# Kernel tuning notes

Hardware: AMD Instinct MI355X
Metric: run time of the kernel (lower is better)

## Reference

```python
import jax, jax.numpy as jnp
import numpy as np

B, S, H, F, E, R, K = 2, 1024, 2048, 7168, 8, 32, 2


def setup_inputs() -> dict:
    key = jax.random.key(0)
    ks = jax.random.split(key, 12)
    sc = 0.02
    n = lambda k, shape, s: jax.random.normal(k, shape, dtype=jnp.float32) * s
    return {
        "hidden_states": n(ks[0], (B, S, H), 1.0),
        "Wg": n(ks[1], (E, H), sc),          # gate: Linear(H, E)
        "W1": n(ks[2], (F, H), sc),          # shared gate_proj
        "W2": n(ks[3], (H, F), sc),          # shared down_proj
        "W3": n(ks[4], (F, H), sc),          # shared up_proj
        "A1": n(ks[5], (E, R, H), sc),       # per-expert w1_a
        "B1": n(ks[6], (E, F, R), sc),       # per-expert w1_b
        "A2": n(ks[7], (E, R, F), sc),       # per-expert w2_a
        "B2": n(ks[8], (E, H, R), sc),       # per-expert w2_b
        "A3": n(ks[9], (E, R, H), sc),       # per-expert w3_a
        "B3": n(ks[10], (E, F, R), sc),      # per-expert w3_b
    }


def _gather_slot(a_all, e):
    # a_all: [T, E, r], e: [T] -> [T, r]
    return jnp.take_along_axis(a_all, e[:, None, None], axis=1)[:, 0]


def reference(hidden_states, Wg, W1, W2, W3, A1, B1, A2, B2, A3, B3):
    b, s, h = hidden_states.shape
    x = hidden_states.reshape(-1, h)                      # [T, H]
    nE = Wg.shape[0]
    logits = x @ Wg.T                                     # [T, E]
    probs = jax.nn.softmax(logits.astype(jnp.float32), axis=-1)
    rw, sel = jax.lax.top_k(probs, K)                     # [T, K]
    rw = (rw / rw.sum(axis=-1, keepdims=True)).astype(x.dtype)

    # Base projections are shared across experts -> compute once for all tokens.
    base1 = x @ W1.T                                      # [T, F]
    base3 = x @ W3.T                                      # [T, F]
    # Tiny per-expert LoRA down-projections for all tokens ([T, E, R]).
    a1_all = jnp.einsum('th,erh->ter', x, A1)
    a3_all = jnp.einsum('th,erh->ter', x, A3)

    out = jnp.zeros_like(x)
    for k in range(K):  # fixed small loop over top-k slots
        e = sel[:, k]                                     # [T]
        mask = jax.nn.one_hot(e, nE, dtype=x.dtype)       # [T, E]
        a1 = _gather_slot(a1_all, e)                      # [T, R]
        a3 = _gather_slot(a3_all, e)
        lora1 = jnp.einsum('ter,efr->tf', mask[:, :, None] * a1[:, None, :], B1)
        lora3 = jnp.einsum('ter,efr->tf', mask[:, :, None] * a3[:, None, :], B3)
        x1 = base1 + lora1
        x3 = base3 + lora3
        x2 = jax.nn.silu(x1) * x3                         # [T, F]
        down = x2 @ W2.T                                  # [T, H]
        a2_all = jnp.einsum('tf,erf->ter', x2, A2)        # [T, E, R]
        a2 = _gather_slot(a2_all, e)
        lora2 = jnp.einsum('ter,ehr->th', mask[:, :, None] * a2[:, None, :], B2)
        out = out + (down + lora2) * rw[:, k:k+1]
    return out.reshape(b, s, h)
```

## Files before the change

### kernel.cpp

```cpp
#include <hip/hip_runtime.h>

typedef unsigned short u16;
typedef unsigned int u32;
typedef __attribute__((ext_vector_type(4))) float f32x4;
typedef __attribute__((ext_vector_type(8))) short short8;

constexpr int TT = 2048;
constexpr int HH = 2048;
constexpr int FF = 7168;
constexpr int RR = 32;
constexpr int KT = 2;
constexpr int NA1 = FF + 256;
constexpr int NA2 = HH + 256;

__device__ __forceinline__ float bf2f(u16 v) {
  union { u32 u; float f; } w; w.u = ((u32)v) << 16; return w.f;
}
__device__ __forceinline__ u16 f2bf(float f) {
  union { float f; u32 u; } w; w.f = f;
  u32 u = w.u;
  return (u16)((u + 0x7FFFu + ((u >> 16) & 1u)) >> 16);
}

__device__ __forceinline__ void gload16(const u16* g, u16* l) {
  __builtin_amdgcn_global_load_lds(
      (__attribute__((address_space(1))) void*)g,
      (__attribute__((address_space(3))) void*)l, 16, 0, 0);
}

__device__ __forceinline__ void bar_mem() { asm volatile("s_barrier" ::: "memory"); }
__device__ __forceinline__ void lgk0() { asm volatile("s_waitcnt lgkmcnt(0)" ::: "memory"); }
template <int N>
__device__ __forceinline__ void vmw() { asm volatile("s_waitcnt vmcnt(%0)" :: "n"(N) : "memory"); }

__global__ __launch_bounds__(256) void cvt_kernel(
    const float* __restrict__ src, u16* __restrict__ dst, int n4) {
  int stride = gridDim.x * 256;
  for (int i = blockIdx.x * 256 + threadIdx.x; i < n4; i += stride) {
    float4 v = ((const float4*)src)[i];
    ushort4 o;
    o.x = f2bf(v.x); o.y = f2bf(v.y); o.z = f2bf(v.z); o.w = f2bf(v.w);
    ((ushort4*)dst)[i] = o;
  }
}

__global__ __launch_bounds__(256) void repackB_kernel(
    const float* __restrict__ B, u16* __restrict__ Bm, int Fdim) {
  int n = Fdim * 256;
  int stride = gridDim.x * 256;
  for (int i = blockIdx.x * 256 + threadIdx.x; i < n; i += stride) {
    int f = i >> 8, c = i & 255, e = c >> 5, r = c & 31;
    Bm[i] = f2bf(B[((size_t)e * Fdim + f) * RR + r]);
  }
}

__global__ __launch_bounds__(64) void gating_kernel(
    const float* __restrict__ X, const float* __restrict__ Wg,
    int* __restrict__ sel, float* __restrict__ rw) {
  int t = blockIdx.x;
  int lane = threadIdx.x;
  const float* x = X + (size_t)t * HH;
  float acc[8] = {};
  for (int h = lane; h < HH; h += 64) {
    float xv = x[h];
#pragma unroll
    for (int e = 0; e < 8; e++) acc[e] += xv * Wg[e * HH + h];
  }
#pragma unroll
  for (int e = 0; e < 8; e++)
    for (int off = 32; off; off >>= 1) acc[e] += __shfl_down(acc[e], off);
  if (lane == 0) {
    int b0 = 0; float l0 = acc[0];
    for (int e = 1; e < 8; e++) if (acc[e] > l0) { l0 = acc[e]; b0 = e; }
    int b1 = -1; float l1 = 0.f;
    for (int e = 0; e < 8; e++) {
      if (e == b0) continue;
      if (b1 < 0 || acc[e] > l1) { l1 = acc[e]; b1 = e; }
    }
    float p = 1.f / (1.f + __expf(l1 - l0));
    sel[t * 2 + 0] = b0; sel[t * 2 + 1] = b1;
    rw[t * 2 + 0] = p;   rw[t * 2 + 1] = 1.f - p;
  }
}

__device__ __forceinline__ void stageH(const u16* g, int stride, int row0, int k0,
                                       u16* l) {
  const int tid = threadIdx.x;
#pragma unroll
  for (int j = 0; j < 2; ++j) {
    int c = (j << 9) + tid;
    int row = c >> 3, c8 = c & 7;
    int sc = ((c8 ^ (row & 7)) << 3);
    gload16(g + (size_t)(row0 + row) * stride + (k0 + sc), l + c * 8);
  }
}

#define RD_A(buf, mo)                                                         \
  _Pragma("unroll") for (int j = 0; j < 4; ++j)                               \
  _Pragma("unroll") for (int ks = 0; ks < 2; ++ks) {                          \
    int row = wmw + (mo + j) * 16 + r15;                                      \
    a[j * 2 + ks] = *(const short8*)((buf) + row * 64 +                       \
                                     (((ks * 4 + q) ^ (row & 7)) << 3));      \
  }
#define RD_B(buf, reg, no)                                                    \
  _Pragma("unroll") for (int n = 0; n < 2; ++n)                               \
  _Pragma("unroll") for (int ks = 0; ks < 2; ++ks) {                          \
    int row = wnw + (no + n) * 16 + r15;                                      \
    reg[n * 2 + ks] = *(const short8*)((buf) + row * 64 +                     \
                                       (((ks * 4 + q) ^ (row & 7)) << 3));    \
  }
#define MMQ(mo, reg, no)                                                      \
  _Pragma("unroll") for (int m = 0; m < 4; ++m)                               \
  _Pragma("unroll") for (int n = 0; n < 2; ++n)                               \
  _Pragma("unroll") for (int ks = 0; ks < 2; ++ks)                            \
    acc[mo + m][no + n] = __builtin_amdgcn_mfma_f32_16x16x32_bf16(            \
        a[m * 2 + ks], reg[n * 2 + ks], acc[mo + m][no + n], 0, 0, 0);

__global__ __launch_bounds__(512, 2) void gemm256(
    const u16* A0, const u16* A1p, const u16* B0, const u16* B1p,
    u16* Cb0, u16* Cb1, int N, int Kd) {
  const u16* A  = blockIdx.z ? A1p : A0;
  const u16* Bm = blockIdx.z ? B1p : B0;
  u16* Cb       = blockIdx.z ? Cb1 : Cb0;

  __shared__ __align__(16) u16 S[65536];
  u16* A0b = S;
  u16* B0b = S + 16384;
  u16* A1b = S + 32768;
  u16* B1b = S + 49152;

  const int gx = gridDim.x, gy = gridDim.y;
  const int nwg = gx * gy;
  const int orig = blockIdx.y * gx + blockIdx.x;
  const int wg = (orig & 7) * (nwg >> 3) + (orig >> 3);
  const int tn = (wg / gy) * 256;
  const int tm = (wg % gy) * 256;

  const int tid = threadIdx.x;
  const int lane = tid & 63, wave = tid >> 6;
  const int wmw = (wave >> 2) * 128;
  const int wnw = (wave & 3) * 64;
  const int r15 = lane & 15, q = lane >> 4;

  f32x4 acc[8][4] = {};
  short8 a[8], bl[4], bh[4];

  const int nIter = Kd >> 7;

  stageH(A,  Kd, tm,       0,  A0b);
  stageH(A,  Kd, tm + 128, 0,  A0b + 8192);
  stageH(Bm, Kd, tn,       0,  B0b);
  stageH(Bm, Kd, tn + 128, 0,  B0b + 8192);
  stageH(Bm, Kd, tn,       64, B1b);
  stageH(Bm, Kd, tn + 128, 64, B1b + 8192);
  vmw<4>();
  bar_mem();

  for (int it = 0; it < nIter; ++it) {
    const bool st = (it + 1 < nIter);
    const int k1 = (2 * it + 1) << 6;
    const int k2 = (2 * it + 2) << 6;
    const int k3 = (2 * it + 3) << 6;

    RD_A(A0b, 0) RD_B(B0b, bl, 0)
    stageH(A, Kd, tm, k1, A1b);
    bar_mem(); lgk0();
    __builtin_amdgcn_s_setprio(1); MMQ(0, bl, 0) __builtin_amdgcn_s_setprio(0);
    lgk0(); bar_mem();
    RD_B(B0b, bh, 2)
    stageH(A, Kd, tm + 128, k1, A1b + 8192);
    bar_mem(); lgk0();
    __builtin_amdgcn_s_setprio(1); MMQ(0, bh, 2) __builtin_amdgcn_s_setprio(0);
    lgk0(); bar_mem();
    RD_A(A0b, 4)
    if (st) stageH(Bm, Kd, tn, k2, B0b);
    bar_mem(); lgk0();
    __builtin_amdgcn_s_setprio(1); MMQ(4, bh, 2) __builtin_amdgcn_s_setprio(0);
    lgk0(); bar_mem();
    if (st) stageH(Bm, Kd, tn + 128, k2, B0b + 8192);
    bar_mem();
    __builtin_amdgcn_s_setprio(1); MMQ(4, bl, 0) __builtin_amdgcn_s_setprio(0);
    if (st) vmw<4>(); else vmw<0>();
    lgk0(); bar_mem();

    RD_A(A1b, 0) RD_B(B1b, bl, 0)
    if (st) stageH(A, Kd, tm, k2, A0b);
    bar_mem(); lgk0();
    __builtin_amdgcn_s_setprio(1); MMQ(0, bl, 0) __builtin_amdgcn_s_setprio(0);
    lgk0(); bar_mem();
    RD_B(B1b, bh, 2)
    if (st) stageH(A, Kd, tm + 128, k2, A0b + 8192);
    bar_mem(); lgk0();
    __builtin_amdgcn_s_setprio(1); MMQ(0, bh, 2) __builtin_amdgcn_s_setprio(0);
    lgk0(); bar_mem();
    RD_A(A1b, 4)
    if (st) stageH(Bm, Kd, tn, k3, B1b);
    bar_mem(); lgk0();
    __builtin_amdgcn_s_setprio(1); MMQ(4, bh, 2) __builtin_amdgcn_s_setprio(0);
    lgk0(); bar_mem();
    if (st) stageH(Bm, Kd, tn + 128, k3, B1b + 8192);
    bar_mem();
    __builtin_amdgcn_s_setprio(1); MMQ(4, bl, 0) __builtin_amdgcn_s_setprio(0);
    if (st) vmw<4>();
    lgk0(); bar_mem();
  }

#pragma unroll
  for (int m = 0; m < 8; ++m)
#pragma unroll
    for (int n = 0; n < 4; ++n)
#pragma unroll
      for (int i = 0; i < 4; ++i) {
        int r = tm + wmw + m * 16 + q * 4 + i;
        int cc = tn + wnw + n * 16 + r15;
        Cb[(size_t)r * N + cc] = f2bf(acc[m][n][i]);
      }
}

__global__ __launch_bounds__(256) void gemm_bt(
    const u16* A0, const u16* A1p,
    const u16* B0, const u16* B1p,
    u16* Cb0, u16* Cb1, float* Cf0, float* Cf1,
    int N, int Kd, int out_bf16) {
  const u16* A  = blockIdx.z ? A1p : A0;
  const u16* Bm = blockIdx.z ? B1p : B0;
  u16* Cb       = blockIdx.z ? Cb1 : Cb0;
  float* Cf     = blockIdx.z ? Cf1 : Cf0;

  __shared__ __align__(16) u16 As[128 * 64];
  __shared__ __align__(16) u16 Bs[128 * 64];

  int tid = threadIdx.x;
  int tn = blockIdx.x * 128;
  int tm = blockIdx.y * 128;
  int lane = tid & 63;
  int wave = tid >> 6;
  int wm = (wave >> 1) * 64, wn = (wave & 1) * 64;
  const int r15 = lane & 15, q = lane >> 4;

  f32x4 acc[4][4] = {};

  for (int k0 = 0; k0 < Kd; k0 += 64) {
#pragma unroll
    for (int it = 0; it < 4; it++) {
      int c = it * 256 + tid;
      int row = c >> 3, c8 = c & 7;
      int scol = ((c8 ^ (row & 7)) << 3);
      gload16(A + (size_t)(tm + row) * Kd + (k0 + scol), As + c * 8);
      gload16(Bm + (size_t)(tn + row) * Kd + (k0 + scol), Bs + c * 8);
    }
    __syncthreads();
#pragma unroll
    for (int kk = 0; kk < 2; kk++) {
      short8 af[4], bfr[4];
#pragma unroll
      for (int mi = 0; mi < 4; mi++) {
        int row = wm + mi * 16 + r15;
        int kc = (kk * 4 + q) ^ (row & 7);
        af[mi] = *(const short8*)(As + row * 64 + kc * 8);
      }
#pragma unroll
      for (int ni = 0; ni < 4; ni++) {
        int row = wn + ni * 16 + r15;
        int kc = (kk * 4 + q) ^ (row & 7);
        bfr[ni] = *(const short8*)(Bs + row * 64 + kc * 8);
      }
#pragma unroll
      for (int mi = 0; mi < 4; mi++)
#pragma unroll
        for (int ni = 0; ni < 4; ni++)
          acc[mi][ni] = __builtin_amdgcn_mfma_f32_16x16x32_bf16(af[mi], bfr[ni], acc[mi][ni], 0, 0, 0);
    }
    __syncthreads();
  }
#pragma unroll
  for (int mi = 0; mi < 4; mi++)
#pragma unroll
    for (int ni = 0; ni < 4; ni++)
#pragma unroll
      for (int i = 0; i < 4; i++) {
        int r = tm + wm + mi * 16 + q * 4 + i;
        int cc = tn + wn + ni * 16 + r15;
        float v = acc[mi][ni][i];
        if (out_bf16) Cb[(size_t)r * N + cc] = f2bf(v);
        else          Cf[(size_t)r * N + cc] = v;
      }
}

__global__ __launch_bounds__(256) void mask13_kernel(
    const u16* __restrict__ Y1, const u16* __restrict__ Y3,
    const int* __restrict__ sel, u16* __restrict__ ah1, u16* __restrict__ ah3) {
  int tk = blockIdx.x;
  int t = tk >> 1;
  int e = sel[tk] & 7;
  int c = threadIdx.x;
  bool in = (c >> 5) == e;
  ah1[(size_t)tk * 256 + c] = in ? Y1[(size_t)t * NA1 + FF + c] : (u16)0;
  ah3[(size_t)tk * 256 + c] = in ? Y3[(size_t)t * NA1 + FF + c] : (u16)0;
}

__global__ __launch_bounds__(256) void mask2_kernel(
    const u16* __restrict__ down_aug, const int* __restrict__ sel,
    u16* __restrict__ ah2) {
  int tk = blockIdx.x;
  int t = tk >> 1, k = tk & 1;
  int e = sel[tk] & 7;
  int c = threadIdx.x;
  ah2[(size_t)tk * 256 + c] =
      ((c >> 5) == e) ? down_aug[((size_t)k * TT + t) * NA2 + HH + c] : (u16)0;
}

__global__ __launch_bounds__(256) void lora_silu_kernel(
    const u16* __restrict__ ah1, const u16* __restrict__ ah3,
    const u16* __restrict__ Bm1, const u16* __restrict__ Bm3,
    const u16* __restrict__ Y1, const u16* __restrict__ Y3,
    u16* __restrict__ X2) {
  __shared__ __align__(16) u16 Bs1[128 * 64];
  __shared__ __align__(16) u16 Bs3[128 * 64];
  int tid = threadIdx.x;
  int tn = blockIdx.x * 128;
  int tm = blockIdx.y * 128;
  int lane = tid & 63, wave = tid >> 6;
  int wm = (wave >> 1) * 64, wn = (wave & 1) * 64;
  const int r15 = lane & 15, q = lane >> 4;

  f32x4 acc1[4][4] = {}, acc3[4][4] = {};

  for (int k0 = 0; k0 < 256; k0 += 64) {
#pragma unroll
    for (int it = 0; it < 4; it++) {
      int c = it * 256 + tid;
      int row = c >> 3, c8 = c & 7;
      int scol = ((c8 ^ (row & 7)) << 3);
      gload16(Bm1 + (size_t)(tn + row) * 256 + (k0 + scol), Bs1 + c * 8);
      gload16(Bm3 + (size_t)(tn + row) * 256 + (k0 + scol), Bs3 + c * 8);
    }
    __syncthreads();
#pragma unroll
    for (int kk = 0; kk < 2; kk++) {
      short8 a1f[4], a3f[4], b1f[4], b3f[4];
#pragma unroll
      for (int mi = 0; mi < 4; mi++) {
        int row = tm + wm + mi * 16 + r15;
        size_t o = (size_t)row * 256 + k0 + (kk * 4 + q) * 8;
        a1f[mi] = *(const short8*)(ah1 + o);
        a3f[mi] = *(const short8*)(ah3 + o);
      }
#pragma unroll
      for (int ni = 0; ni < 4; ni++) {
        int row = wn + ni * 16 + r15;
        int kc = (kk * 4 + q) ^ (row & 7);
        b1f[ni] = *(const short8*)(Bs1 + row * 64 + kc * 8);
        b3f[ni] = *(const short8*)(Bs3 + row * 64 + kc * 8);
      }
#pragma unroll
      for (int mi = 0; mi < 4; mi++)
#pragma unroll
        for (int ni = 0; ni < 4; ni++) {
          acc1[mi][ni] = __builtin_amdgcn_mfma_f32_16x16x32_bf16(a1f[mi], b1f[ni], acc1[mi][ni], 0, 0, 0);
          acc3[mi][ni] = __builtin_amdgcn_mfma_f32_16x16x32_bf16(a3f[mi], b3f[ni], acc3[mi][ni], 0, 0, 0);
        }
    }
    __syncthreads();
  }
#pragma unroll
  for (int mi = 0; mi < 4; mi++)
#pragma unroll
    for (int ni = 0; ni < 4; ni++)
#pragma unroll
      for (int i = 0; i < 4; i++) {
        int row = tm + wm + mi * 16 + q * 4 + i;
        int f = tn + wn + ni * 16 + r15;
        int t = row >> 1, k = row & 1;
        float x1 = bf2f(Y1[(size_t)t * NA1 + f]) + acc1[mi][ni][i];
        float x3 = bf2f(Y3[(size_t)t * NA1 + f]) + acc3[mi][ni][i];
        float sig = 1.f / (1.f + __expf(-x1));
        X2[((size_t)k * TT + t) * FF + f] = f2bf(x1 * sig * x3);
      }
}

__global__ __launch_bounds__(256) void final_kernel(
    const u16* __restrict__ down_aug, const float* __restrict__ L2b,
    const float* __restrict__ rw, float* __restrict__ out) {
  int t = blockIdx.x;
  float r0 = rw[t * 2], r1 = rw[t * 2 + 1];
  int h = threadIdx.x * 8;
  short8 d0v = *(const short8*)(down_aug + (size_t)t * NA2 + h);
  short8 d1v = *(const short8*)(down_aug + ((size_t)TT + t) * NA2 + h);
  const float* l0p = L2b + (size_t)(t * 2) * HH + h;
  const float* l1p = L2b + (size_t)(t * 2 + 1) * HH + h;
  f32x4 l0a = *(const f32x4*)(l0p),     l0b = *(const f32x4*)(l0p + 4);
  f32x4 l1a = *(const f32x4*)(l1p),     l1b = *(const f32x4*)(l1p + 4);
  f32x4 oa, ob;
#pragma unroll
  for (int j = 0; j < 4; j++) {
    oa[j] = r0 * (bf2f((u16)d0v[j])     + l0a[j]) + r1 * (bf2f((u16)d1v[j])     + l1a[j]);
    ob[j] = r0 * (bf2f((u16)d0v[j + 4]) + l0b[j]) + r1 * (bf2f((u16)d1v[j + 4]) + l1b[j]);
  }
  float* op = out + (size_t)t * HH + h;
  *(f32x4*)(op)     = oa;
  *(f32x4*)(op + 4) = ob;
}

extern "C" void kernel_launch(void* const* d_in, const int* in_sizes, int n_in,
                              void* d_out, int out_size, void* d_ws, size_t ws_size,
                              hipStream_t stream) {
  if (n_in < 11) return;
  const float* X  = (const float*)d_in[0];
  const float* Wg = (const float*)d_in[1];
  const float* W1 = (const float*)d_in[2];
  const float* W2 = (const float*)d_in[3];
  const float* W3 = (const float*)d_in[4];
  const float* A1 = (const float*)d_in[5];
  const float* B1 = (const float*)d_in[6];
  const float* A2 = (const float*)d_in[7];
  const float* B2 = (const float*)d_in[8];
  const float* A3 = (const float*)d_in[9];
  const float* B3 = (const float*)d_in[10];
  float* out = (float*)d_out;

  char* ws = (char*)d_ws;
  size_t off = 0;
  auto take = [&](size_t bytes) -> void* {
    void* p = ws + off;
    off += (bytes + 255) & ~(size_t)255;
    return p;
  };
  u16*   Xb     = (u16*)take((size_t)TT * HH * 2);
  u16*   W1augb = (u16*)take((size_t)NA1 * HH * 2);
  u16*   W3augb = (u16*)take((size_t)NA1 * HH * 2);
  u16*   W2augb = (u16*)take((size_t)NA2 * FF * 2);
  u16*   Bm1    = (u16*)take((size_t)FF * 256 * 2);
  u16*   Bm3    = (u16*)take((size_t)FF * 256 * 2);
  u16*   Bm2    = (u16*)take((size_t)HH * 256 * 2);
  u16*   Y1aug  = (u16*)take((size_t)TT * NA1 * 2);
  u16*   Y3aug  = (u16*)take((size_t)TT * NA1 * 2);
  u16*   ah1    = (u16*)take((size_t)TT * KT * 256 * 2);
  u16*   ah3    = (u16*)take((size_t)TT * KT * 256 * 2);
  u16*   ah2    = (u16*)take((size_t)TT * KT * 256 * 2);
  u16*   X2     = (u16*)take((size_t)KT * TT * FF * 2);
  int*   sel    = (int*)take((size_t)TT * KT * 4);
  float* rw     = (float*)take((size_t)TT * KT * 4);
  if (off > ws_size) return;
  u16*   down_aug = W1augb;
  float* L2b      = (float*)W3augb;

  cvt_kernel<<<1024, 256, 0, stream>>>(X,  Xb, TT * HH / 4);
  cvt_kernel<<<1024, 256, 0, stream>>>(W1, W1augb, FF * HH / 4);
  cvt_kernel<<<1024, 256, 0, stream>>>(A1, W1augb + (size_t)FF * HH, 256 * HH / 4);
  cvt_kernel<<<1024, 256, 0, stream>>>(W3, W3augb, FF * HH / 4);
  cvt_kernel<<<1024, 256, 0, stream>>>(A3, W3augb + (size_t)FF * HH, 256 * HH / 4);
  cvt_kernel<<<1024, 256, 0, stream>>>(W2, W2augb, HH * FF / 4);
  cvt_kernel<<<1024, 256, 0, stream>>>(A2, W2augb + (size_t)HH * FF, 256 * FF / 4);
  repackB_kernel<<<1024, 256, 0, stream>>>(B1, Bm1, FF);
  repackB_kernel<<<1024, 256, 0, stream>>>(B3, Bm3, FF);
  repackB_kernel<<<1024, 256, 0, stream>>>(B2, Bm2, HH);
  gating_kernel<<<TT, 64, 0, stream>>>(X, Wg, sel, rw);

  gemm256<<<dim3(NA1 / 256, TT / 256, 2), 512, 0, stream>>>(
      Xb, Xb, W1augb, W3augb, Y1aug, Y3aug, NA1, HH);
  mask13_kernel<<<TT * KT, 256, 0, stream>>>(Y1aug, Y3aug, sel, ah1, ah3);
  lora_silu_kernel<<<dim3(FF / 128, TT * KT / 128), 256, 0, stream>>>(
      ah1, ah3, Bm1, Bm3, Y1aug, Y3aug, X2);
  gemm256<<<dim3(NA2 / 256, TT / 256, 2), 512, 0, stream>>>(
      X2, X2 + (size_t)TT * FF, W2augb, W2augb,
      down_aug, down_aug + (size_t)TT * NA2, NA2, FF);
  mask2_kernel<<<TT * KT, 256, 0, stream>>>(down_aug, sel, ah2);
  gemm_bt<<<dim3(HH / 128, TT * KT / 128, 1), 256, 0, stream>>>(
      ah2, ah2, Bm2, Bm2, nullptr, nullptr, L2b, L2b, HH, 256, 0);
  final_kernel<<<TT, 256, 0, stream>>>(down_aug, L2b, rw, out);
}
```

Baseline: 704.2 us.

## Triple-buffer A tiles in LDS to prefetch two K-steps ahead

The 256x256 GEMM now keeps three rotating LDS buffers for the A operand instead of two. This lets A loads for the K-step after next be issued earlier, and the vmcnt wait threshold is raised to match. It also drops several lgkmcnt waits after MFMA groups, so less time is spent stalled on outstanding LDS reads. In exchange, LDS per block grows to 160 KB, the full CU budget, which rules out any co-resident block or extra shared memory.

```diff
diff --git a/kernel.cpp b/kernel.cpp
--- a/kernel.cpp
+++ b/kernel.cpp
@@ -123,11 +123,12 @@
   const u16* Bm = blockIdx.z ? B1p : B0;
   u16* Cb       = blockIdx.z ? Cb1 : Cb0;
 
-  __shared__ __align__(16) u16 S[65536];
-  u16* A0b = S;
-  u16* B0b = S + 16384;
-  u16* A1b = S + 32768;
-  u16* B1b = S + 49152;
+  __shared__ __align__(16) u16 S[81920];
+  u16* Acur  = S;
+  u16* Anext = S + 16384;
+  u16* Afree = S + 32768;
+  u16* B0b   = S + 49152;
+  u16* B1b   = S + 65536;
 
   const int gx = gridDim.x, gy = gridDim.y;
   const int nwg = gx * gy;
@@ -147,62 +148,65 @@
 
   const int nIter = Kd >> 7;
 
-  stageH(A,  Kd, tm,       0,  A0b);
-  stageH(A,  Kd, tm + 128, 0,  A0b + 8192);
+  stageH(A,  Kd, tm,       0,  Acur);
+  stageH(A,  Kd, tm + 128, 0,  Acur + 8192);
   stageH(Bm, Kd, tn,       0,  B0b);
   stageH(Bm, Kd, tn + 128, 0,  B0b + 8192);
+  stageH(A,  Kd, tm,       64, Anext);
+  stageH(A,  Kd, tm + 128, 64, Anext + 8192);
   stageH(Bm, Kd, tn,       64, B1b);
   stageH(Bm, Kd, tn + 128, 64, B1b + 8192);
-  vmw<4>();
+  vmw<8>();
   bar_mem();
 
   for (int it = 0; it < nIter; ++it) {
     const bool st = (it + 1 < nIter);
-    const int k1 = (2 * it + 1) << 6;
     const int k2 = (2 * it + 2) << 6;
     const int k3 = (2 * it + 3) << 6;
 
-    RD_A(A0b, 0) RD_B(B0b, bl, 0)
-    stageH(A, Kd, tm, k1, A1b);
+    RD_A(Acur, 0) RD_B(B0b, bl, 0)
+    if (st) stageH(A, Kd, tm, k2, Afree);
     bar_mem(); lgk0();
     __builtin_amdgcn_s_setprio(1); MMQ(0, bl, 0) __builtin_amdgcn_s_setprio(0);
-    lgk0(); bar_mem();
+    bar_mem();
     RD_B(B0b, bh, 2)
-    stageH(A, Kd, tm + 128, k1, A1b + 8192);
+    if (st) stageH(A, Kd, tm + 128, k2, Afree + 8192);
     bar_mem(); lgk0();
     __builtin_amdgcn_s_setprio(1); MMQ(0, bh, 2) __builtin_amdgcn_s_setprio(0);
-    lgk0(); bar_mem();
-    RD_A(A0b, 4)
+    bar_mem();
+    RD_A(Acur, 4)
     if (st) stageH(Bm, Kd, tn, k2, B0b);
     bar_mem(); lgk0();
     __builtin_amdgcn_s_setprio(1); MMQ(4, bh, 2) __builtin_amdgcn_s_setprio(0);
-    lgk0(); bar_mem();
+    bar_mem();
     if (st) stageH(Bm, Kd, tn + 128, k2, B0b + 8192);
     bar_mem();
     __builtin_amdgcn_s_setprio(1); MMQ(4, bl, 0) __builtin_amdgcn_s_setprio(0);
-    if (st) vmw<4>(); else vmw<0>();
-    lgk0(); bar_mem();
-
-    RD_A(A1b, 0) RD_B(B1b, bl, 0)
-    if (st) stageH(A, Kd, tm, k2, A0b);
+    if (st) vmw<8>(); else vmw<0>();
+    bar_mem();
+
+    RD_A(Anext, 0) RD_B(B1b, bl, 0)
+    if (st) stageH(A, Kd, tm, k3, Acur);
     bar_mem(); lgk0();
     __builtin_amdgcn_s_setprio(1); MMQ(0, bl, 0) __builtin_amdgcn_s_setprio(0);
-    lgk0(); bar_mem();
+    bar_mem();
     RD_B(B1b, bh, 2)
-    if (st) stageH(A, Kd, tm + 128, k2, A0b + 8192);
+    if (st) stageH(A, Kd, tm + 128, k3, Acur + 8192);
     bar_mem(); lgk0();
     __builtin_amdgcn_s_setprio(1); MMQ(0, bh, 2) __builtin_amdgcn_s_setprio(0);
-    lgk0(); bar_mem();
-    RD_A(A1b, 4)
+    bar_mem();
+    RD_A(Anext, 4)
     if (st) stageH(Bm, Kd, tn, k3, B1b);
     bar_mem(); lgk0();
     __builtin_amdgcn_s_setprio(1); MMQ(4, bh, 2) __builtin_amdgcn_s_setprio(0);
-    lgk0(); bar_mem();
+    bar_mem();
     if (st) stageH(Bm, Kd, tn + 128, k3, B1b + 8192);
     bar_mem();
     __builtin_amdgcn_s_setprio(1); MMQ(4, bl, 0) __builtin_amdgcn_s_setprio(0);
-    if (st) vmw<4>();
-    lgk0(); bar_mem();
+    if (st) vmw<8>();
+    bar_mem();
+
+    u16* tmp = Afree; Afree = Anext; Anext = Acur; Acur = tmp;
   }
 
 #pragma unroll
```

Result: no change. 701.3 us (-0.4%).

## Replace async LDS-direct GEMM pipeline with register-staged double buffering; fuse conversions

Applied to the files above, without the earlier changes.

The main 256x256 GEMM drops the global_load_lds direct-to-LDS staging and its fine-grained barrier choreography. It now loads the next K=64 tile into registers, writes it to the alternate LDS buffer, and uses a single barrier per 64-wide K step. The seven separate fp32-to-bf16 conversion launches are merged into one grid-stride prep kernel. The GEMM change trades async LDS loads for extra VGPR usage (8 uint4 per thread) and explicit LDS writes, which may add register pressure at 512 threads with 2 blocks per CU.

```diff
diff --git a/kernel.cpp b/kernel.cpp
--- a/kernel.cpp
+++ b/kernel.cpp
@@ -30,17 +30,35 @@
 
 __device__ __forceinline__ void bar_mem() { asm volatile("s_barrier" ::: "memory"); }
 __device__ __forceinline__ void lgk0() { asm volatile("s_waitcnt lgkmcnt(0)" ::: "memory"); }
-template <int N>
-__device__ __forceinline__ void vmw() { asm volatile("s_waitcnt vmcnt(%0)" :: "n"(N) : "memory"); }
-
-__global__ __launch_bounds__(256) void cvt_kernel(
-    const float* __restrict__ src, u16* __restrict__ dst, int n4) {
+
+__global__ __launch_bounds__(256) void prep_kernel(
+    const float* __restrict__ X,  u16* __restrict__ Xb,
+    const float* __restrict__ W1, const float* __restrict__ A1, u16* __restrict__ W1augb,
+    const float* __restrict__ W3, const float* __restrict__ A3, u16* __restrict__ W3augb,
+    const float* __restrict__ W2, const float* __restrict__ A2, u16* __restrict__ W2augb) {
+  constexpr int n0 = TT * HH / 4;
+  constexpr int n1 = FF * HH / 4;
+  constexpr int n2 = 256 * HH / 4;
+  constexpr int n3 = FF * HH / 4;
+  constexpr int n4 = 256 * HH / 4;
+  constexpr int n5 = HH * FF / 4;
+  constexpr int n6 = 256 * FF / 4;
+  constexpr int c0 = n0, c1 = c0 + n1, c2 = c1 + n2, c3 = c2 + n3,
+                c4 = c3 + n4, c5 = c4 + n5, c6 = c5 + n6;
   int stride = gridDim.x * 256;
-  for (int i = blockIdx.x * 256 + threadIdx.x; i < n4; i += stride) {
-    float4 v = ((const float4*)src)[i];
+  for (int i = blockIdx.x * 256 + threadIdx.x; i < c6; i += stride) {
+    const float* src; u16* dst; int j;
+    if (i < c0)      { src = X;  dst = Xb;                          j = i; }
+    else if (i < c1) { src = W1; dst = W1augb;                      j = i - c0; }
+    else if (i < c2) { src = A1; dst = W1augb + (size_t)FF * HH;    j = i - c1; }
+    else if (i < c3) { src = W3; dst = W3augb;                      j = i - c2; }
+    else if (i < c4) { src = A3; dst = W3augb + (size_t)FF * HH;    j = i - c3; }
+    else if (i < c5) { src = W2; dst = W2augb;                      j = i - c4; }
+    else             { src = A2; dst = W2augb + (size_t)HH * FF;    j = i - c5; }
+    float4 v = ((const float4*)src)[j];
     ushort4 o;
     o.x = f2bf(v.x); o.y = f2bf(v.y); o.z = f2bf(v.z); o.w = f2bf(v.w);
-    ((ushort4*)dst)[i] = o;
+    ((ushort4*)dst)[j] = o;
   }
 }
 
@@ -83,18 +101,20 @@
   }
 }
 
-__device__ __forceinline__ void stageH(const u16* g, int stride, int row0, int k0,
-                                       u16* l) {
-  const int tid = threadIdx.x;
-#pragma unroll
-  for (int j = 0; j < 2; ++j) {
-    int c = (j << 9) + tid;
-    int row = c >> 3, c8 = c & 7;
-    int sc = ((c8 ^ (row & 7)) << 3);
-    gload16(g + (size_t)(row0 + row) * stride + (k0 + sc), l + c * 8);
-  }
-}
-
+#define LOADT(k0)                                                             \
+  _Pragma("unroll") for (int j = 0; j < 4; ++j) {                             \
+    int c = (j << 9) + tid;                                                   \
+    int row = c >> 3, c8 = c & 7;                                             \
+    int sc = ((c8 ^ (row & 7)) << 3);                                         \
+    ra[j] = *(const uint4*)(A + (size_t)(tm + row) * Kd + ((k0) + sc));       \
+    rb[j] = *(const uint4*)(Bm + (size_t)(tn + row) * Kd + ((k0) + sc));      \
+  }
+#define WRITET(Ab, Bb)                                                        \
+  _Pragma("unroll") for (int j = 0; j < 4; ++j) {                             \
+    int c = (j << 9) + tid;                                                   \
+    *(uint4*)((Ab) + c * 8) = ra[j];                                          \
+    *(uint4*)((Bb) + c * 8) = rb[j];                                          \
+  }
 #define RD_A(buf, mo)                                                         \
   _Pragma("unroll") for (int j = 0; j < 4; ++j)                               \
   _Pragma("unroll") for (int ks = 0; ks < 2; ++ks) {                          \
@@ -124,10 +144,10 @@
   u16* Cb       = blockIdx.z ? Cb1 : Cb0;
 
   __shared__ __align__(16) u16 S[65536];
-  u16* A0b = S;
-  u16* B0b = S + 16384;
-  u16* A1b = S + 32768;
-  u16* B1b = S + 49152;
+  u16* Acur = S;
+  u16* Bcur = S + 16384;
+  u16* Anxt = S + 32768;
+  u16* Bnxt = S + 49152;
 
   const int gx = gridDim.x, gy = gridDim.y;
   const int nwg = gx * gy;
@@ -144,65 +164,31 @@
 
   f32x4 acc[8][4] = {};
   short8 a[8], bl[4], bh[4];
-
-  const int nIter = Kd >> 7;
-
-  stageH(A,  Kd, tm,       0,  A0b);
-  stageH(A,  Kd, tm + 128, 0,  A0b + 8192);
-  stageH(Bm, Kd, tn,       0,  B0b);
-  stageH(Bm, Kd, tn + 128, 0,  B0b + 8192);
-  stageH(Bm, Kd, tn,       64, B1b);
-  stageH(Bm, Kd, tn + 128, 64, B1b + 8192);
-  vmw<4>();
-  bar_mem();
+  uint4 ra[4], rb[4];
+
+  const int nIter = Kd >> 6;
+
+  LOADT(0)
+  WRITET(Acur, Bcur)
+  LOADT(64)
+  lgk0(); bar_mem();
 
   for (int it = 0; it < nIter; ++it) {
-    const bool st = (it + 1 < nIter);
-    const int k1 = (2 * it + 1) << 6;
-    const int k2 = (2 * it + 2) << 6;
-    const int k3 = (2 * it + 3) << 6;
-
-    RD_A(A0b, 0) RD_B(B0b, bl, 0)
-    stageH(A, Kd, tm, k1, A1b);
-    bar_mem(); lgk0();
+    if (it + 1 < nIter) {
+      WRITET(Anxt, Bnxt)
+      if (it + 2 < nIter) { LOADT((it + 2) << 6) }
+    }
+    RD_A(Acur, 0) RD_B(Bcur, bl, 0)
     __builtin_amdgcn_s_setprio(1); MMQ(0, bl, 0) __builtin_amdgcn_s_setprio(0);
-    lgk0(); bar_mem();
-    RD_B(B0b, bh, 2)
-    stageH(A, Kd, tm + 128, k1, A1b + 8192);
-    bar_mem(); lgk0();
+    RD_B(Bcur, bh, 2)
     __builtin_amdgcn_s_setprio(1); MMQ(0, bh, 2) __builtin_amdgcn_s_setprio(0);
-    lgk0(); bar_mem();
-    RD_A(A0b, 4)
-    if (st) stageH(Bm, Kd, tn, k2, B0b);
-    bar_mem(); lgk0();
-    __builtin_amdgcn_s_setprio(1); MMQ(4, bh, 2) __builtin_amdgcn_s_setprio(0);
-    lgk0(); bar_mem();
-    if (st) stageH(Bm, Kd, tn + 128, k2, B0b + 8192);
+    RD_A(Acur, 4)
+    __builtin_amdgcn_s_setprio(1); MMQ(4, bh, 2) MMQ(4, bl, 0) __builtin_amdgcn_s_setprio(0);
+    lgk0();
     bar_mem();
-    __builtin_amdgcn_s_setprio(1); MMQ(4, bl, 0) __builtin_amdgcn_s_setprio(0);
-    if (st) vmw<4>(); else vmw<0>();
-    lgk0(); bar_mem();
-
-    RD_A(A1b, 0) RD_B(B1b, bl, 0)
-    if (st) stageH(A, Kd, tm, k2, A0b);
-    bar_mem(); lgk0();
-    __builtin_amdgcn_s_setprio(1); MMQ(0, bl, 0) __builtin_amdgcn_s_setprio(0);
-    lgk0(); bar_mem();
-    RD_B(B1b, bh, 2)
-    if (st) stageH(A, Kd, tm + 128, k2, A0b + 8192);
-    bar_mem(); lgk0();
-    __builtin_amdgcn_s_setprio(1); MMQ(0, bh, 2) __builtin_amdgcn_s_setprio(0);
-    lgk0(); bar_mem();
-    RD_A(A1b, 4)
-    if (st) stageH(Bm, Kd, tn, k3, B1b);
-    bar_mem(); lgk0();
-    __builtin_amdgcn_s_setprio(1); MMQ(4, bh, 2) __builtin_amdgcn_s_setprio(0);
-    lgk0(); bar_mem();
-    if (st) stageH(Bm, Kd, tn + 128, k3, B1b + 8192);
-    bar_mem();
-    __builtin_amdgcn_s_setprio(1); MMQ(4, bl, 0) __builtin_amdgcn_s_setprio(0);
-    if (st) vmw<4>();
-    lgk0(); bar_mem();
+    u16* t;
+    t = Acur; Acur = Anxt; Anxt = t;
+    t = Bcur; Bcur = Bnxt; Bnxt = t;
   }
 
 #pragma unroll
@@ -445,13 +431,8 @@
   u16*   down_aug = W1augb;
   float* L2b      = (float*)W3augb;
 
-  cvt_kernel<<<1024, 256, 0, stream>>>(X,  Xb, TT * HH / 4);
-  cvt_kernel<<<1024, 256, 0, stream>>>(W1, W1augb, FF * HH / 4);
-  cvt_kernel<<<1024, 256, 0, stream>>>(A1, W1augb + (size_t)FF * HH, 256 * HH / 4);
-  cvt_kernel<<<1024, 256, 0, stream>>>(W3, W3augb, FF * HH / 4);
-  cvt_kernel<<<1024, 256, 0, stream>>>(A3, W3augb + (size_t)FF * HH, 256 * HH / 4);
-  cvt_kernel<<<1024, 256, 0, stream>>>(W2, W2augb, HH * FF / 4);
-  cvt_kernel<<<1024, 256, 0, stream>>>(A2, W2augb + (size_t)HH * FF, 256 * FF / 4);
+  prep_kernel<<<2048, 256, 0, stream>>>(X, Xb, W1, A1, W1augb, W3, A3, W3augb,
+                                        W2, A2, W2augb);
   repackB_kernel<<<1024, 256, 0, stream>>>(B1, Bm1, FF);
   repackB_kernel<<<1024, 256, 0, stream>>>(B3, Bm3, FF);
   repackB_kernel<<<1024, 256, 0, stream>>>(B2, Bm2, HH);
```

New measurement: 1.155 ms. +64.0%, slower.
